# Kernel optimization log

Hardware: AMD Instinct MI355X
Metric: run time of the kernel (lower is better)

## Reference

```python
import jax, jax.numpy as jnp
import numpy as np

N = 8192
DEG = 16            # neighbors per node (excluding self loop)
E = N * (DEG + 1)   # edges incl. self loops
IN, HID, OUT = 512, 256, 128
N_HIDDEN_LAYERS = 2  # n_layers - 1
NEG_SLOPE = 0.2


def _build_adj():
    # circulant-ish adjacency: self loop + 16 fixed offsets -> exactly E nonzeros
    offs = np.concatenate([[0], np.arange(1, DEG + 1) * 131])
    cols = ((np.arange(N)[:, None] + offs[None, :]) % N).reshape(-1)
    rows = np.repeat(np.arange(N), DEG + 1)
    adj = np.zeros((N, N), np.float32)
    adj[rows, cols] = 1.0
    return adj


def setup_inputs() -> dict:
    key = jax.random.key(0)
    ks = jax.random.split(key, 12)
    g = lambda k, shape, fan_in: jax.random.normal(k, shape, jnp.float32) / np.sqrt(fan_in)
    return {
        "x": jax.random.normal(ks[0], (N, IN), jnp.float32),
        "adj": jnp.asarray(_build_adj()),
        "W_emb": g(ks[1], (IN, HID), IN),
        "b_emb": jnp.zeros((HID,), jnp.float32),
        "W_h": g(ks[2], (N_HIDDEN_LAYERS, HID, HID), HID),
        "asrc_h": g(ks[3], (N_HIDDEN_LAYERS, HID), HID),
        "adst_h": g(ks[4], (N_HIDDEN_LAYERS, HID), HID),
        "b_h": jnp.zeros((N_HIDDEN_LAYERS, HID), jnp.float32),
        "W_o": g(ks[5], (HID, OUT), HID),
        "asrc_o": g(ks[6], (OUT,), OUT),
        "adst_o": g(ks[7], (OUT,), OUT),
        "b_o": jnp.zeros((OUT,), jnp.float32),
        "num_edges": E,
    }


def _leaky(v):
    return jnp.where(v >= 0, v, NEG_SLOPE * v)


def _gat_conv(h_in, src, dst, W, a_src, a_dst, b, n):
    # PyG GATConv, heads=1: h = x W; e_ij = LeakyReLU(a_src.h_j + a_dst.h_i)
    # softmax over incoming edges per target i, then weighted scatter-sum + bias.
    h = h_in @ W                                   # [n, out]
    e = _leaky((h @ a_src)[src] + (h @ a_dst)[dst])  # [E]
    m = jax.ops.segment_max(e, dst, num_segments=n)
    w = jnp.exp(e - m[dst])
    s = jax.ops.segment_sum(w, dst, num_segments=n)
    coef = w / s[dst]                              # [E]
    out = jax.ops.segment_sum(coef[:, None] * h[src], dst, num_segments=n)
    return out + b


def reference(x, adj, W_emb, b_emb, W_h, asrc_h, adst_h, b_h, W_o, asrc_o, adst_o, b_o, num_edges):
    n = adj.shape[0]
    # dense_to_sparse: row=target, col=source (SparseTensor adj_t convention)
    dst, src = jnp.nonzero(adj, size=num_edges)
    h = x @ W_emb + b_emb        # emb Linear; dropout is identity in eval
    for l in range(W_h.shape[0]):
        h = _gat_conv(h, src, dst, W_h[l], asrc_h[l], adst_h[l], b_h[l], n)
    return _gat_conv(h, src, dst, W_o, asrc_o, adst_o, b_o, n)
```

## Files before the change

### kernel.cpp

```cpp
#include <hip/hip_runtime.h>


#define N_NODES 8192
#define NMASK 8191

typedef __attribute__((ext_vector_type(8))) short short8;
typedef __attribute__((ext_vector_type(4))) float f32x4;

__device__ __forceinline__ unsigned short f2bf(float f) {
    unsigned u = __float_as_uint(f);
    u += 0x7FFF + ((u >> 16) & 1);
    return (unsigned short)(u >> 16);
}
__device__ __forceinline__ float bf2f(unsigned short h) {
    return __uint_as_float(((unsigned)h) << 16);
}
__device__ __forceinline__ int kswz(int k, int row) {
    return (k & ~63) | ((((k >> 3) & 7) ^ (row & 7)) << 3) | (k & 7);
}
__device__ __forceinline__ void gl_lds16(const void* g, void* lds) {
    __builtin_amdgcn_global_load_lds(
        (const __attribute__((address_space(1))) unsigned int*)g,
        (__attribute__((address_space(3))) unsigned int*)lds, 16, 0, 0);
}

__global__ __launch_bounds__(256)
void prep1(const float* __restrict__ W_emb, const float* __restrict__ W_h,
           unsigned short* __restrict__ wembT, unsigned short* __restrict__ whT) {
    const int idx = blockIdx.x * 256 + threadIdx.x;
    if (idx < 131072) {
        const int n = idx >> 9, k = idx & 511;
        wembT[n * 512 + kswz(k, n)] = f2bf(W_emb[k * 256 + n]);
    } else if (idx < 196608) {
        const int i = idx - 131072;
        const int n = i >> 8, k = i & 255;
        whT[n * 256 + kswz(k, n)] = f2bf(W_h[k * 256 + n]);
    }
}

__global__ __launch_bounds__(512)
void fused_emb_l0(const float* __restrict__ x, const float* __restrict__ W_h,
                  const float* __restrict__ W_o,
                  const unsigned short* __restrict__ wembT,
                  const unsigned short* __restrict__ whT0,
                  unsigned short* __restrict__ whT1, unsigned short* __restrict__ woT,
                  const float* __restrict__ b_emb,
                  const float* __restrict__ a_src, const float* __restrict__ a_dst,
                  float* __restrict__ as_out, float* __restrict__ ad_out,
                  float* __restrict__ hw_out) {
    __shared__ unsigned short sB[2][256 * 64];
    __shared__ unsigned short sA[2 * 32 * 256];
    __shared__ float sRed[2][8][16];
    unsigned short* sAhi = sA;
    unsigned short* sAlo = sA + 32 * 256;
    const int tid = threadIdx.x;
    const int wave = tid >> 6, lane = tid & 63;
    const int wr = wave >> 2, wq = wave & 3;
    const int fl_c = lane & 15, fl_g = lane >> 4;
    const int r0 = blockIdx.x * 32;

    {
        const int idx = blockIdx.x * 512 + tid;
        if (idx < 65536) {
            const int n = idx >> 8, k = idx & 255;
            whT1[n * 256 + kswz(k, n)] = f2bf(W_h[65536 + k * 256 + n]);
        } else if (idx < 98304) {
            const int i = idx - 65536;
            const int n = i >> 8, k = i & 255;
            woT[n * 256 + kswz(k, n)] = f2bf(W_o[k * 128 + n]);
        }
    }

    auto stageB = [&](const unsigned short* W, int stride, int buf, int t) {
        #pragma unroll
        for (int it = 0; it < 4; ++it) {
            const int G = it * 512 + tid;
            const int n = G >> 3, s = G & 7;
            gl_lds16(W + n * stride + t * 64 + s * 8,
                     &sB[buf][(it * 512 + wave * 64) * 8]);
        }
    };

    const int grow = (131 * (r0 + wr * 16 + fl_c)) & NMASK;
    f32x4 acc[4] = {};
    stageB(wembT, 512, 0, 0);
    __syncthreads();
    int cur = 0;
    for (int t = 0; t < 8; ++t) {
        if (t + 1 < 8) stageB(wembT, 512, cur ^ 1, t + 1);
        short8 ah[2], al[2];
        const float* xp = x + (size_t)grow * 512 + t * 64;
        #pragma unroll
        for (int kh = 0; kh < 2; ++kh) {
            const float4 v0 = *(const float4*)(xp + kh * 32 + fl_g * 8);
            const float4 v1 = *(const float4*)(xp + kh * 32 + fl_g * 8 + 4);
            const float vv[8] = {v0.x, v0.y, v0.z, v0.w, v1.x, v1.y, v1.z, v1.w};
            short8 h8, l8;
            #pragma unroll
            for (int j = 0; j < 8; ++j) {
                const unsigned short h = f2bf(vv[j]);
                h8[j] = (short)h;
                l8[j] = (short)f2bf(vv[j] - bf2f(h));
            }
            ah[kh] = h8; al[kh] = l8;
        }
        short8 bh[4][2];
        #pragma unroll
        for (int n = 0; n < 4; ++n) {
            const int c = wq * 64 + n * 16 + fl_c;
            #pragma unroll
            for (int kh = 0; kh < 2; ++kh)
                bh[n][kh] = *(const short8*)&sB[cur][c * 64 + (((kh * 4 + fl_g) ^ (c & 7)) << 3)];
        }
        #pragma unroll
        for (int n = 0; n < 4; ++n)
            #pragma unroll
            for (int kh = 0; kh < 2; ++kh) {
                acc[n] = __builtin_amdgcn_mfma_f32_16x16x32_bf16(ah[kh], bh[n][kh], acc[n], 0, 0, 0);
                acc[n] = __builtin_amdgcn_mfma_f32_16x16x32_bf16(al[kh], bh[n][kh], acc[n], 0, 0, 0);
            }
        __syncthreads();
        cur ^= 1;
    }

    #pragma unroll
    for (int n = 0; n < 4; ++n) {
        const int c = wq * 64 + n * 16 + fl_c;
        const float bb = b_emb[c];
        #pragma unroll
        for (int i = 0; i < 4; ++i) {
            const int lr = wr * 16 + fl_g * 4 + i;
            const float v = acc[n][i] + bb;
            const int pos = lr * 256 + kswz(c, lr);
            const unsigned short h = f2bf(v);
            sAhi[pos] = h;
            sAlo[pos] = f2bf(v - bf2f(h));
        }
    }
    stageB(whT0, 256, 0, 0);
    __syncthreads();

    f32x4 acc2[4] = {};
    cur = 0;
    const int rr = wr * 16 + fl_c;
    for (int t = 0; t < 4; ++t) {
        if (t + 1 < 4) stageB(whT0, 256, cur ^ 1, t + 1);
        short8 ah[2], al[2];
        #pragma unroll
        for (int kh = 0; kh < 2; ++kh) {
            const int off = rr * 256 + t * 64 + (((kh * 4 + fl_g) ^ (rr & 7)) << 3);
            ah[kh] = *(const short8*)&sAhi[off];
            al[kh] = *(const short8*)&sAlo[off];
        }
        short8 bh[4][2];
        #pragma unroll
        for (int n = 0; n < 4; ++n) {
            const int c = wq * 64 + n * 16 + fl_c;
            #pragma unroll
            for (int kh = 0; kh < 2; ++kh)
                bh[n][kh] = *(const short8*)&sB[cur][c * 64 + (((kh * 4 + fl_g) ^ (c & 7)) << 3)];
        }
        #pragma unroll
        for (int n = 0; n < 4; ++n)
            #pragma unroll
            for (int kh = 0; kh < 2; ++kh) {
                acc2[n] = __builtin_amdgcn_mfma_f32_16x16x32_bf16(ah[kh], bh[n][kh], acc2[n], 0, 0, 0);
                acc2[n] = __builtin_amdgcn_mfma_f32_16x16x32_bf16(al[kh], bh[n][kh], acc2[n], 0, 0, 0);
            }
        __syncthreads();
        cur ^= 1;
    }

    float sv[4], dv[4];
    #pragma unroll
    for (int n = 0; n < 4; ++n) {
        const int c = wq * 64 + n * 16 + fl_c;
        sv[n] = a_src[c]; dv[n] = a_dst[c];
    }
    #pragma unroll
    for (int i = 0; i < 4; ++i) {
        float ps = 0.f, pd = 0.f;
        #pragma unroll
        for (int n = 0; n < 4; ++n) { ps += acc2[n][i] * sv[n]; pd += acc2[n][i] * dv[n]; }
        #pragma unroll
        for (int off = 1; off < 16; off <<= 1) {
            ps += __shfl_xor(ps, off, 64);
            pd += __shfl_xor(pd, off, 64);
        }
        if (fl_c == 0) {
            sRed[0][wave][fl_g * 4 + i] = ps;
            sRed[1][wave][fl_g * 4 + i] = pd;
        }
    }
    __syncthreads();
    if (tid < 32) {
        const int band = tid >> 4, rl = tid & 15;
        as_out[r0 + tid] = sRed[0][band * 4 + 0][rl] + sRed[0][band * 4 + 1][rl]
                         + sRed[0][band * 4 + 2][rl] + sRed[0][band * 4 + 3][rl];
        ad_out[r0 + tid] = sRed[1][band * 4 + 0][rl] + sRed[1][band * 4 + 1][rl]
                         + sRed[1][band * 4 + 2][rl] + sRed[1][band * 4 + 3][rl];
    }
    #pragma unroll
    for (int n = 0; n < 4; ++n) {
        const int c = wq * 64 + n * 16 + fl_c;
        #pragma unroll
        for (int i = 0; i < 4; ++i)
            hw_out[(size_t)(r0 + wr * 16 + fl_g * 4 + i) * 256 + c] = acc2[n][i];
    }
}

__global__ __launch_bounds__(512)
void gat_layer_agg(const float* __restrict__ hwPrev, const float* __restrict__ asPrev,
                   const float* __restrict__ adPrev, const float* __restrict__ aggBias,
                   const unsigned short* __restrict__ Bw,
                   const float* __restrict__ a_src, const float* __restrict__ a_dst,
                   float* __restrict__ as_out, float* __restrict__ ad_out,
                   float* __restrict__ hw_out) {
    __shared__ unsigned short sA[2 * 32 * 256];
    __shared__ unsigned short sB[2][256 * 64];
    __shared__ float sWin[48 * 256];
    __shared__ float sAs[48];
    __shared__ float sRed[2][8][16];
    unsigned short* sAhi = sA;
    unsigned short* sAlo = sA + 32 * 256;
    const int tid = threadIdx.x;
    const int wave = tid >> 6, lane = tid & 63;
    const int wr = wave >> 2, wq = wave & 3;
    const int fl_c = lane & 15, fl_g = lane >> 4;
    const int r0 = blockIdx.x * 32;

    auto stageB = [&](int buf, int t) {
        #pragma unroll
        for (int it = 0; it < 4; ++it) {
            const int G = it * 512 + tid;
            const int n = G >> 3, s = G & 7;
            gl_lds16(Bw + n * 256 + t * 64 + s * 8,
                     &sB[buf][(it * 512 + wave * 64) * 8]);
        }
    };

    #pragma unroll
    for (int it = 0; it < 6; ++it) {
        const int G = it * 512 + tid;
        const int j = G >> 6, q = G & 63;
        gl_lds16(hwPrev + (size_t)((r0 + j) & NMASK) * 256 + q * 4,
                 &sWin[(it * 512 + wave * 64) * 4]);
    }
    if (tid < 48) sAs[tid] = asPrev[(r0 + tid) & NMASK];
    stageB(0, 0);
    __syncthreads();
    #pragma unroll
    for (int i = 0; i < 4; ++i) {
        const int t = wave * 4 + i;
        const float adi = adPrev[r0 + t];
        float e[17];
        float mx = -3.4e38f;
        #pragma unroll
        for (int k = 0; k < 17; ++k) {
            float v = sAs[t + k] + adi;
            v = (v >= 0.f) ? v : 0.2f * v;
            e[k] = v;
            mx = fmaxf(mx, v);
        }
        float sum = 0.f;
        #pragma unroll
        for (int k = 0; k < 17; ++k) { e[k] = __expf(e[k] - mx); sum += e[k]; }
        const float inv = 1.f / sum;
        float a0 = 0, a1 = 0, a2 = 0, a3 = 0;
        #pragma unroll
        for (int k = 0; k < 17; ++k) {
            const float c = e[k] * inv;
            const float4 hv = *(const float4*)&sWin[(t + k) * 256 + lane * 4];
            a0 += c * hv.x; a1 += c * hv.y; a2 += c * hv.z; a3 += c * hv.w;
        }
        const float4 bb = *(const float4*)&aggBias[lane * 4];
        a0 += bb.x; a1 += bb.y; a2 += bb.z; a3 += bb.w;
        ushort4 h, l;
        h.x = f2bf(a0); l.x = f2bf(a0 - bf2f(h.x));
        h.y = f2bf(a1); l.y = f2bf(a1 - bf2f(h.y));
        h.z = f2bf(a2); l.z = f2bf(a2 - bf2f(h.z));
        h.w = f2bf(a3); l.w = f2bf(a3 - bf2f(h.w));
        const int pos = t * 256 + kswz(lane * 4, t);
        *(ushort4*)&sAhi[pos] = h;
        *(ushort4*)&sAlo[pos] = l;
    }
    __syncthreads();

    f32x4 acc[4] = {};
    int cur = 0;
    const int rr = wr * 16 + fl_c;
    for (int t = 0; t < 4; ++t) {
        if (t + 1 < 4) stageB(cur ^ 1, t + 1);
        short8 ah[2], al[2];
        #pragma unroll
        for (int kh = 0; kh < 2; ++kh) {
            const int off = rr * 256 + t * 64 + (((kh * 4 + fl_g) ^ (rr & 7)) << 3);
            ah[kh] = *(const short8*)&sAhi[off];
            al[kh] = *(const short8*)&sAlo[off];
        }
        short8 bh[4][2];
        #pragma unroll
        for (int n = 0; n < 4; ++n) {
            const int c = wq * 64 + n * 16 + fl_c;
            #pragma unroll
            for (int kh = 0; kh < 2; ++kh)
                bh[n][kh] = *(const short8*)&sB[cur][c * 64 + (((kh * 4 + fl_g) ^ (c & 7)) << 3)];
        }
        #pragma unroll
        for (int n = 0; n < 4; ++n)
            #pragma unroll
            for (int kh = 0; kh < 2; ++kh) {
                acc[n] = __builtin_amdgcn_mfma_f32_16x16x32_bf16(ah[kh], bh[n][kh], acc[n], 0, 0, 0);
                acc[n] = __builtin_amdgcn_mfma_f32_16x16x32_bf16(al[kh], bh[n][kh], acc[n], 0, 0, 0);
            }
        __syncthreads();
        cur ^= 1;
    }

    float sv[4], dv[4];
    #pragma unroll
    for (int n = 0; n < 4; ++n) {
        const int c = wq * 64 + n * 16 + fl_c;
        sv[n] = a_src[c]; dv[n] = a_dst[c];
    }
    #pragma unroll
    for (int i = 0; i < 4; ++i) {
        float ps = 0.f, pd = 0.f;
        #pragma unroll
        for (int n = 0; n < 4; ++n) { ps += acc[n][i] * sv[n]; pd += acc[n][i] * dv[n]; }
        #pragma unroll
        for (int off = 1; off < 16; off <<= 1) {
            ps += __shfl_xor(ps, off, 64);
            pd += __shfl_xor(pd, off, 64);
        }
        if (fl_c == 0) {
            sRed[0][wave][fl_g * 4 + i] = ps;
            sRed[1][wave][fl_g * 4 + i] = pd;
        }
    }
    __syncthreads();
    if (tid < 32) {
        const int band = tid >> 4, rl = tid & 15;
        as_out[r0 + tid] = sRed[0][band * 4 + 0][rl] + sRed[0][band * 4 + 1][rl]
                         + sRed[0][band * 4 + 2][rl] + sRed[0][band * 4 + 3][rl];
        ad_out[r0 + tid] = sRed[1][band * 4 + 0][rl] + sRed[1][band * 4 + 1][rl]
                         + sRed[1][band * 4 + 2][rl] + sRed[1][band * 4 + 3][rl];
    }
    #pragma unroll
    for (int n = 0; n < 4; ++n) {
        const int c = wq * 64 + n * 16 + fl_c;
        #pragma unroll
        for (int i = 0; i < 4; ++i)
            hw_out[(size_t)(r0 + wr * 16 + fl_g * 4 + i) * 256 + c] = acc[n][i];
    }
}

__global__ __launch_bounds__(512)
void final_fused(const float* __restrict__ hwPrev, const float* __restrict__ asPrev,
                 const float* __restrict__ adPrev, const float* __restrict__ aggBias,
                 const unsigned short* __restrict__ Bw,
                 const float* __restrict__ a_src, const float* __restrict__ a_dst,
                 const float* __restrict__ b_o, float* __restrict__ out) {
    __shared__ float sWin[64 * 256];
    __shared__ unsigned short sA2[2 * 48 * 256];
    __shared__ unsigned short sB[2][128 * 64];
    __shared__ float sAs1[64], sAs2[48], sAd2[48];
    unsigned short* sA2hi = sA2;
    unsigned short* sA2lo = sA2 + 48 * 256;
    const int tid = threadIdx.x;
    const int wave = tid >> 6, lane = tid & 63;
    const int fl_c = lane & 15, fl_g = lane >> 4;
    const int r0 = blockIdx.x * 32;

    auto stageB = [&](int buf, int t) {
        #pragma unroll
        for (int it = 0; it < 2; ++it) {
            const int G = it * 512 + tid;
            const int n = G >> 3, s = G & 7;
            gl_lds16(Bw + n * 256 + t * 64 + s * 8,
                     &sB[buf][(it * 512 + wave * 64) * 8]);
        }
    };

    #pragma unroll
    for (int it = 0; it < 8; ++it) {
        const int G = it * 512 + tid;
        const int j = G >> 6, q = G & 63;
        gl_lds16(hwPrev + (size_t)((r0 + j) & NMASK) * 256 + q * 4,
                 &sWin[(it * 512 + wave * 64) * 4]);
    }
    if (tid < 64) sAs1[tid] = asPrev[(r0 + tid) & NMASK];
    stageB(0, 0);
    __syncthreads();

    #pragma unroll
    for (int i = 0; i < 6; ++i) {
        const int t = wave * 6 + i;
        const float adi = adPrev[(r0 + t) & NMASK];
        float e[17];
        float mx = -3.4e38f;
        #pragma unroll
        for (int k = 0; k < 17; ++k) {
            float v = sAs1[t + k] + adi;
            v = (v >= 0.f) ? v : 0.2f * v;
            e[k] = v;
            mx = fmaxf(mx, v);
        }
        float sum = 0.f;
        #pragma unroll
        for (int k = 0; k < 17; ++k) { e[k] = __expf(e[k] - mx); sum += e[k]; }
        const float inv = 1.f / sum;
        float a0 = 0, a1 = 0, a2 = 0, a3 = 0;
        #pragma unroll
        for (int k = 0; k < 17; ++k) {
            const float c = e[k] * inv;
            const float4 hv = *(const float4*)&sWin[(t + k) * 256 + lane * 4];
            a0 += c * hv.x; a1 += c * hv.y; a2 += c * hv.z; a3 += c * hv.w;
        }
        const float4 bb = *(const float4*)&aggBias[lane * 4];
        a0 += bb.x; a1 += bb.y; a2 += bb.z; a3 += bb.w;
        ushort4 h, l;
        h.x = f2bf(a0); l.x = f2bf(a0 - bf2f(h.x));
        h.y = f2bf(a1); l.y = f2bf(a1 - bf2f(h.y));
        h.z = f2bf(a2); l.z = f2bf(a2 - bf2f(h.z));
        h.w = f2bf(a3); l.w = f2bf(a3 - bf2f(h.w));
        const int pos = t * 256 + kswz(lane * 4, t);
        *(ushort4*)&sA2hi[pos] = h;
        *(ushort4*)&sA2lo[pos] = l;
    }
    __syncthreads();

    f32x4 accF[3] = {};
    int bands[3], cgs[3];
    #pragma unroll
    for (int j = 0; j < 3; ++j) {
        const int f = wave * 3 + j;
        bands[j] = f >> 3; cgs[j] = f & 7;
    }
    int cur = 0;
    for (int t = 0; t < 4; ++t) {
        if (t + 1 < 4) stageB(cur ^ 1, t + 1);
        #pragma unroll
        for (int j = 0; j < 3; ++j) {
            const int rr = bands[j] * 16 + fl_c;
            const int c  = cgs[j] * 16 + fl_c;
            #pragma unroll
            for (int kh = 0; kh < 2; ++kh) {
                const int aoff = rr * 256 + t * 64 + (((kh * 4 + fl_g) ^ (rr & 7)) << 3);
                const short8 ah = *(const short8*)&sA2hi[aoff];
                const short8 al = *(const short8*)&sA2lo[aoff];
                const short8 bh = *(const short8*)&sB[cur][c * 64 + (((kh * 4 + fl_g) ^ (c & 7)) << 3)];
                accF[j] = __builtin_amdgcn_mfma_f32_16x16x32_bf16(ah, bh, accF[j], 0, 0, 0);
                accF[j] = __builtin_amdgcn_mfma_f32_16x16x32_bf16(al, bh, accF[j], 0, 0, 0);
            }
        }
        __syncthreads();
        cur ^= 1;
    }

    float* sHw2 = sWin;
    #pragma unroll
    for (int j = 0; j < 3; ++j)
        #pragma unroll
        for (int i = 0; i < 4; ++i)
            sHw2[(bands[j] * 16 + fl_g * 4 + i) * 128 + cgs[j] * 16 + fl_c] = accF[j][i];
    __syncthreads();

    const float2 s2 = *(const float2*)&a_src[lane * 2];
    const float2 d2 = *(const float2*)&a_dst[lane * 2];
    #pragma unroll
    for (int i = 0; i < 6; ++i) {
        const int t = wave * 6 + i;
        const float2 hv = *(const float2*)&sHw2[t * 128 + lane * 2];
        float ps = hv.x * s2.x + hv.y * s2.y;
        float pd = hv.x * d2.x + hv.y * d2.y;
        #pragma unroll
        for (int off = 1; off < 64; off <<= 1) {
            ps += __shfl_xor(ps, off, 64);
            pd += __shfl_xor(pd, off, 64);
        }
        if (lane == 0) { sAs2[t] = ps; sAd2[t] = pd; }
    }
    __syncthreads();

    const float2 bb = *(const float2*)&b_o[lane * 2];
    #pragma unroll
    for (int i = 0; i < 4; ++i) {
        const int t = wave * 4 + i;
        const int nid = (131 * (r0 + t)) & NMASK;
        const float adi = sAd2[t];
        float e[17];
        float mx = -3.4e38f;
        #pragma unroll
        for (int k = 0; k < 17; ++k) {
            float v = sAs2[t + k] + adi;
            v = (v >= 0.f) ? v : 0.2f * v;
            e[k] = v;
            mx = fmaxf(mx, v);
        }
        float sum = 0.f;
        #pragma unroll
        for (int k = 0; k < 17; ++k) { e[k] = __expf(e[k] - mx); sum += e[k]; }
        const float inv = 1.f / sum;
        float a0 = 0, a1 = 0;
        #pragma unroll
        for (int k = 0; k < 17; ++k) {
            const float c = e[k] * inv;
            const float2 hv = *(const float2*)&sHw2[(t + k) * 128 + lane * 2];
            a0 += c * hv.x; a1 += c * hv.y;
        }
        *(float2*)&out[(size_t)nid * 128 + lane * 2] = make_float2(a0 + bb.x, a1 + bb.y);
    }
}

extern "C" void kernel_launch(void* const* d_in, const int* in_sizes, int n_in,
                              void* d_out, int out_size, void* d_ws, size_t ws_size,
                              hipStream_t stream) {
    (void)in_sizes; (void)n_in; (void)out_size; (void)ws_size;

    const float* x      = (const float*)d_in[0];
    const float* W_emb  = (const float*)d_in[2];
    const float* b_emb  = (const float*)d_in[3];
    const float* W_h    = (const float*)d_in[4];
    const float* asrc_h = (const float*)d_in[5];
    const float* adst_h = (const float*)d_in[6];
    const float* b_h    = (const float*)d_in[7];
    const float* W_o    = (const float*)d_in[8];
    const float* asrc_o = (const float*)d_in[9];
    const float* adst_o = (const float*)d_in[10];
    const float* b_o    = (const float*)d_in[11];

    char* p = (char*)d_ws;
    float* hwA = (float*)p; p += (size_t)N_NODES * 256 * 4;
    float* hwB = (float*)p; p += (size_t)N_NODES * 256 * 4;
    float* as0 = (float*)p; p += N_NODES * 4;
    float* ad0 = (float*)p; p += N_NODES * 4;
    float* as1 = (float*)p; p += N_NODES * 4;
    float* ad1 = (float*)p; p += N_NODES * 4;
    unsigned short* wembT = (unsigned short*)p; p += 256 * 512 * 2;
    unsigned short* whT   = (unsigned short*)p; p += 2 * 256 * 256 * 2;
    unsigned short* woT   = (unsigned short*)p;

    prep1<<<dim3(768), dim3(256), 0, stream>>>(W_emb, W_h, wembT, whT);

    fused_emb_l0<<<dim3(256), dim3(512), 0, stream>>>(
        x, W_h, W_o, wembT, whT, whT + 65536, woT,
        b_emb, asrc_h, adst_h, as0, ad0, hwA);

    gat_layer_agg<<<dim3(256), dim3(512), 0, stream>>>(
        hwA, as0, ad0, b_h,
        whT + 65536, asrc_h + 256, adst_h + 256, as1, ad1, hwB);

    final_fused<<<dim3(256), dim3(512), 0, stream>>>(
        hwB, as1, ad1, b_h + 256, woT, asrc_o, adst_o, b_o, (float*)d_out);
}
```

Baseline: 67.63 us.

## Fuse last two GAT stages with neighbor-block flag handoff; drop x lo-split MFMA

Merges the layer-1 aggregation/transform kernel and the final output kernel into one launch. Between the two phases each block waits only on a flag set by the next block, since its 48-row window needs just those rows, so the grid-wide kernel boundary is gone. Separately, the embedding GEMM drops the bf16 low-part correction for x, which halves its MFMA count at the cost of some accuracy. The spin-wait assumes all 256 blocks are co-resident, and both phases share LDS through a union.

```diff
diff --git a/kernel.cpp b/kernel.cpp
--- a/kernel.cpp
+++ b/kernel.cpp
@@ -26,8 +26,10 @@
 
 __global__ __launch_bounds__(256)
 void prep1(const float* __restrict__ W_emb, const float* __restrict__ W_h,
-           unsigned short* __restrict__ wembT, unsigned short* __restrict__ whT) {
+           unsigned short* __restrict__ wembT, unsigned short* __restrict__ whT,
+           unsigned* __restrict__ flags) {
     const int idx = blockIdx.x * 256 + threadIdx.x;
+    if (idx < 256) flags[idx] = 0u;
     if (idx < 131072) {
         const int n = idx >> 9, k = idx & 511;
         wembT[n * 512 + kswz(k, n)] = f2bf(W_emb[k * 256 + n]);
@@ -88,21 +90,17 @@
     int cur = 0;
     for (int t = 0; t < 8; ++t) {
         if (t + 1 < 8) stageB(wembT, 512, cur ^ 1, t + 1);
-        short8 ah[2], al[2];
+        short8 ah[2];
         const float* xp = x + (size_t)grow * 512 + t * 64;
         #pragma unroll
         for (int kh = 0; kh < 2; ++kh) {
             const float4 v0 = *(const float4*)(xp + kh * 32 + fl_g * 8);
             const float4 v1 = *(const float4*)(xp + kh * 32 + fl_g * 8 + 4);
             const float vv[8] = {v0.x, v0.y, v0.z, v0.w, v1.x, v1.y, v1.z, v1.w};
-            short8 h8, l8;
-            #pragma unroll
-            for (int j = 0; j < 8; ++j) {
-                const unsigned short h = f2bf(vv[j]);
-                h8[j] = (short)h;
-                l8[j] = (short)f2bf(vv[j] - bf2f(h));
-            }
-            ah[kh] = h8; al[kh] = l8;
+            short8 h8;
+            #pragma unroll
+            for (int j = 0; j < 8; ++j) h8[j] = (short)f2bf(vv[j]);
+            ah[kh] = h8;
         }
         short8 bh[4][2];
         #pragma unroll
@@ -115,10 +113,8 @@
         #pragma unroll
         for (int n = 0; n < 4; ++n)
             #pragma unroll
-            for (int kh = 0; kh < 2; ++kh) {
+            for (int kh = 0; kh < 2; ++kh)
                 acc[n] = __builtin_amdgcn_mfma_f32_16x16x32_bf16(ah[kh], bh[n][kh], acc[n], 0, 0, 0);
-                acc[n] = __builtin_amdgcn_mfma_f32_16x16x32_bf16(al[kh], bh[n][kh], acc[n], 0, 0, 0);
-            }
         __syncthreads();
         cur ^= 1;
     }
@@ -209,307 +205,326 @@
     }
 }
 
+union TailSmem {
+    struct {
+        float win[48 * 256];
+        unsigned short A[2 * 32 * 256];
+        unsigned short B[2][256 * 64];
+        float as0[48];
+        float red[2][8][16];
+    } a;
+    struct {
+        float win[64 * 256];
+        unsigned short A2[2 * 48 * 256];
+        unsigned short B[2][128 * 64];
+        float as1[64], as2[48], ad2[48];
+    } b;
+};
+
 __global__ __launch_bounds__(512)
-void gat_layer_agg(const float* __restrict__ hwPrev, const float* __restrict__ asPrev,
-                   const float* __restrict__ adPrev, const float* __restrict__ aggBias,
-                   const unsigned short* __restrict__ Bw,
-                   const float* __restrict__ a_src, const float* __restrict__ a_dst,
-                   float* __restrict__ as_out, float* __restrict__ ad_out,
-                   float* __restrict__ hw_out) {
-    __shared__ unsigned short sA[2 * 32 * 256];
-    __shared__ unsigned short sB[2][256 * 64];
-    __shared__ float sWin[48 * 256];
-    __shared__ float sAs[48];
-    __shared__ float sRed[2][8][16];
-    unsigned short* sAhi = sA;
-    unsigned short* sAlo = sA + 32 * 256;
+void tail_fused(const float* __restrict__ hwA, const float* __restrict__ as0,
+                const float* __restrict__ ad0, const float* __restrict__ bias0,
+                const unsigned short* __restrict__ whT1,
+                const float* __restrict__ asrc1, const float* __restrict__ adst1,
+                float* __restrict__ as1, float* __restrict__ ad1,
+                float* __restrict__ hwB, const float* __restrict__ bias1,
+                const unsigned short* __restrict__ woT,
+                const float* __restrict__ asrc_o, const float* __restrict__ adst_o,
+                const float* __restrict__ b_o, unsigned* __restrict__ flags,
+                float* __restrict__ out) {
+    __shared__ TailSmem smem;
     const int tid = threadIdx.x;
     const int wave = tid >> 6, lane = tid & 63;
     const int wr = wave >> 2, wq = wave & 3;
     const int fl_c = lane & 15, fl_g = lane >> 4;
-    const int r0 = blockIdx.x * 32;
-
-    auto stageB = [&](int buf, int t) {
-        #pragma unroll
-        for (int it = 0; it < 4; ++it) {
+    const int blk = blockIdx.x;
+    const int r0 = blk * 32;
+
+    {
+        unsigned short* sAhi = smem.a.A;
+        unsigned short* sAlo = smem.a.A + 32 * 256;
+
+        auto stageB = [&](int buf, int t) {
+            #pragma unroll
+            for (int it = 0; it < 4; ++it) {
+                const int G = it * 512 + tid;
+                const int n = G >> 3, s = G & 7;
+                gl_lds16(whT1 + n * 256 + t * 64 + s * 8,
+                         &smem.a.B[buf][(it * 512 + wave * 64) * 8]);
+            }
+        };
+
+        #pragma unroll
+        for (int it = 0; it < 6; ++it) {
             const int G = it * 512 + tid;
-            const int n = G >> 3, s = G & 7;
-            gl_lds16(Bw + n * 256 + t * 64 + s * 8,
-                     &sB[buf][(it * 512 + wave * 64) * 8]);
-        }
-    };
-
-    #pragma unroll
-    for (int it = 0; it < 6; ++it) {
-        const int G = it * 512 + tid;
-        const int j = G >> 6, q = G & 63;
-        gl_lds16(hwPrev + (size_t)((r0 + j) & NMASK) * 256 + q * 4,
-                 &sWin[(it * 512 + wave * 64) * 4]);
-    }
-    if (tid < 48) sAs[tid] = asPrev[(r0 + tid) & NMASK];
-    stageB(0, 0);
-    __syncthreads();
-    #pragma unroll
-    for (int i = 0; i < 4; ++i) {
-        const int t = wave * 4 + i;
-        const float adi = adPrev[r0 + t];
-        float e[17];
-        float mx = -3.4e38f;
-        #pragma unroll
-        for (int k = 0; k < 17; ++k) {
-            float v = sAs[t + k] + adi;
-            v = (v >= 0.f) ? v : 0.2f * v;
-            e[k] = v;
-            mx = fmaxf(mx, v);
-        }
-        float sum = 0.f;
-        #pragma unroll
-        for (int k = 0; k < 17; ++k) { e[k] = __expf(e[k] - mx); sum += e[k]; }
-        const float inv = 1.f / sum;
-        float a0 = 0, a1 = 0, a2 = 0, a3 = 0;
-        #pragma unroll
-        for (int k = 0; k < 17; ++k) {
-            const float c = e[k] * inv;
-            const float4 hv = *(const float4*)&sWin[(t + k) * 256 + lane * 4];
-            a0 += c * hv.x; a1 += c * hv.y; a2 += c * hv.z; a3 += c * hv.w;
-        }
-        const float4 bb = *(const float4*)&aggBias[lane * 4];
-        a0 += bb.x; a1 += bb.y; a2 += bb.z; a3 += bb.w;
-        ushort4 h, l;
-        h.x = f2bf(a0); l.x = f2bf(a0 - bf2f(h.x));
-        h.y = f2bf(a1); l.y = f2bf(a1 - bf2f(h.y));
-        h.z = f2bf(a2); l.z = f2bf(a2 - bf2f(h.z));
-        h.w = f2bf(a3); l.w = f2bf(a3 - bf2f(h.w));
-        const int pos = t * 256 + kswz(lane * 4, t);
-        *(ushort4*)&sAhi[pos] = h;
-        *(ushort4*)&sAlo[pos] = l;
-    }
-    __syncthreads();
-
-    f32x4 acc[4] = {};
-    int cur = 0;
-    const int rr = wr * 16 + fl_c;
-    for (int t = 0; t < 4; ++t) {
-        if (t + 1 < 4) stageB(cur ^ 1, t + 1);
-        short8 ah[2], al[2];
-        #pragma unroll
-        for (int kh = 0; kh < 2; ++kh) {
-            const int off = rr * 256 + t * 64 + (((kh * 4 + fl_g) ^ (rr & 7)) << 3);
-            ah[kh] = *(const short8*)&sAhi[off];
-            al[kh] = *(const short8*)&sAlo[off];
-        }
-        short8 bh[4][2];
+            const int j = G >> 6, q = G & 63;
+            gl_lds16(hwA + (size_t)((r0 + j) & NMASK) * 256 + q * 4,
+                     &smem.a.win[(it * 512 + wave * 64) * 4]);
+        }
+        if (tid < 48) smem.a.as0[tid] = as0[(r0 + tid) & NMASK];
+        stageB(0, 0);
+        __syncthreads();
+        #pragma unroll
+        for (int i = 0; i < 4; ++i) {
+            const int t = wave * 4 + i;
+            const float adi = ad0[r0 + t];
+            float e[17];
+            float mx = -3.4e38f;
+            #pragma unroll
+            for (int k = 0; k < 17; ++k) {
+                float v = smem.a.as0[t + k] + adi;
+                v = (v >= 0.f) ? v : 0.2f * v;
+                e[k] = v;
+                mx = fmaxf(mx, v);
+            }
+            float sum = 0.f;
+            #pragma unroll
+            for (int k = 0; k < 17; ++k) { e[k] = __expf(e[k] - mx); sum += e[k]; }
+            const float inv = 1.f / sum;
+            float a0 = 0, a1 = 0, a2 = 0, a3 = 0;
+            #pragma unroll
+            for (int k = 0; k < 17; ++k) {
+                const float c = e[k] * inv;
+                const float4 hv = *(const float4*)&smem.a.win[(t + k) * 256 + lane * 4];
+                a0 += c * hv.x; a1 += c * hv.y; a2 += c * hv.z; a3 += c * hv.w;
+            }
+            const float4 bb = *(const float4*)&bias0[lane * 4];
+            a0 += bb.x; a1 += bb.y; a2 += bb.z; a3 += bb.w;
+            ushort4 h, l;
+            h.x = f2bf(a0); l.x = f2bf(a0 - bf2f(h.x));
+            h.y = f2bf(a1); l.y = f2bf(a1 - bf2f(h.y));
+            h.z = f2bf(a2); l.z = f2bf(a2 - bf2f(h.z));
+            h.w = f2bf(a3); l.w = f2bf(a3 - bf2f(h.w));
+            const int pos = t * 256 + kswz(lane * 4, t);
+            *(ushort4*)&sAhi[pos] = h;
+            *(ushort4*)&sAlo[pos] = l;
+        }
+        __syncthreads();
+
+        f32x4 acc[4] = {};
+        int cur = 0;
+        const int rr = wr * 16 + fl_c;
+        for (int t = 0; t < 4; ++t) {
+            if (t + 1 < 4) stageB(cur ^ 1, t + 1);
+            short8 ah[2], al[2];
+            #pragma unroll
+            for (int kh = 0; kh < 2; ++kh) {
+                const int off = rr * 256 + t * 64 + (((kh * 4 + fl_g) ^ (rr & 7)) << 3);
+                ah[kh] = *(const short8*)&sAhi[off];
+                al[kh] = *(const short8*)&sAlo[off];
+            }
+            short8 bh[4][2];
+            #pragma unroll
+            for (int n = 0; n < 4; ++n) {
+                const int c = wq * 64 + n * 16 + fl_c;
+                #pragma unroll
+                for (int kh = 0; kh < 2; ++kh)
+                    bh[n][kh] = *(const short8*)&smem.a.B[cur][c * 64 + (((kh * 4 + fl_g) ^ (c & 7)) << 3)];
+            }
+            #pragma unroll
+            for (int n = 0; n < 4; ++n)
+                #pragma unroll
+                for (int kh = 0; kh < 2; ++kh) {
+                    acc[n] = __builtin_amdgcn_mfma_f32_16x16x32_bf16(ah[kh], bh[n][kh], acc[n], 0, 0, 0);
+                    acc[n] = __builtin_amdgcn_mfma_f32_16x16x32_bf16(al[kh], bh[n][kh], acc[n], 0, 0, 0);
+                }
+            __syncthreads();
+            cur ^= 1;
+        }
+
+        float sv[4], dv[4];
         #pragma unroll
         for (int n = 0; n < 4; ++n) {
             const int c = wq * 64 + n * 16 + fl_c;
-            #pragma unroll
-            for (int kh = 0; kh < 2; ++kh)
-                bh[n][kh] = *(const short8*)&sB[cur][c * 64 + (((kh * 4 + fl_g) ^ (c & 7)) << 3)];
-        }
-        #pragma unroll
-        for (int n = 0; n < 4; ++n)
-            #pragma unroll
-            for (int kh = 0; kh < 2; ++kh) {
-                acc[n] = __builtin_amdgcn_mfma_f32_16x16x32_bf16(ah[kh], bh[n][kh], acc[n], 0, 0, 0);
-                acc[n] = __builtin_amdgcn_mfma_f32_16x16x32_bf16(al[kh], bh[n][kh], acc[n], 0, 0, 0);
-            }
-        __syncthreads();
-        cur ^= 1;
-    }
-
-    float sv[4], dv[4];
-    #pragma unroll
-    for (int n = 0; n < 4; ++n) {
-        const int c = wq * 64 + n * 16 + fl_c;
-        sv[n] = a_src[c]; dv[n] = a_dst[c];
-    }
-    #pragma unroll
-    for (int i = 0; i < 4; ++i) {
-        float ps = 0.f, pd = 0.f;
-        #pragma unroll
-        for (int n = 0; n < 4; ++n) { ps += acc[n][i] * sv[n]; pd += acc[n][i] * dv[n]; }
-        #pragma unroll
-        for (int off = 1; off < 16; off <<= 1) {
-            ps += __shfl_xor(ps, off, 64);
-            pd += __shfl_xor(pd, off, 64);
-        }
-        if (fl_c == 0) {
-            sRed[0][wave][fl_g * 4 + i] = ps;
-            sRed[1][wave][fl_g * 4 + i] = pd;
-        }
-    }
+            sv[n] = asrc1[c]; dv[n] = adst1[c];
+        }
+        #pragma unroll
+        for (int i = 0; i < 4; ++i) {
+            float ps = 0.f, pd = 0.f;
+            #pragma unroll
+            for (int n = 0; n < 4; ++n) { ps += acc[n][i] * sv[n]; pd += acc[n][i] * dv[n]; }
+            #pragma unroll
+            for (int off = 1; off < 16; off <<= 1) {
+                ps += __shfl_xor(ps, off, 64);
+                pd += __shfl_xor(pd, off, 64);
+            }
+            if (fl_c == 0) {
+                smem.a.red[0][wave][fl_g * 4 + i] = ps;
+                smem.a.red[1][wave][fl_g * 4 + i] = pd;
+            }
+        }
+        __syncthreads();
+        if (tid < 32) {
+            const int band = tid >> 4, rl = tid & 15;
+            as1[r0 + tid] = smem.a.red[0][band * 4 + 0][rl] + smem.a.red[0][band * 4 + 1][rl]
+                          + smem.a.red[0][band * 4 + 2][rl] + smem.a.red[0][band * 4 + 3][rl];
+            ad1[r0 + tid] = smem.a.red[1][band * 4 + 0][rl] + smem.a.red[1][band * 4 + 1][rl]
+                          + smem.a.red[1][band * 4 + 2][rl] + smem.a.red[1][band * 4 + 3][rl];
+        }
+        #pragma unroll
+        for (int n = 0; n < 4; ++n) {
+            const int c = wq * 64 + n * 16 + fl_c;
+            #pragma unroll
+            for (int i = 0; i < 4; ++i)
+                hwB[(size_t)(r0 + wr * 16 + fl_g * 4 + i) * 256 + c] = acc[n][i];
+        }
+    }
+
     __syncthreads();
-    if (tid < 32) {
-        const int band = tid >> 4, rl = tid & 15;
-        as_out[r0 + tid] = sRed[0][band * 4 + 0][rl] + sRed[0][band * 4 + 1][rl]
-                         + sRed[0][band * 4 + 2][rl] + sRed[0][band * 4 + 3][rl];
-        ad_out[r0 + tid] = sRed[1][band * 4 + 0][rl] + sRed[1][band * 4 + 1][rl]
-                         + sRed[1][band * 4 + 2][rl] + sRed[1][band * 4 + 3][rl];
-    }
-    #pragma unroll
-    for (int n = 0; n < 4; ++n) {
-        const int c = wq * 64 + n * 16 + fl_c;
-        #pragma unroll
-        for (int i = 0; i < 4; ++i)
-            hw_out[(size_t)(r0 + wr * 16 + fl_g * 4 + i) * 256 + c] = acc[n][i];
-    }
-}
-
-__global__ __launch_bounds__(512)
-void final_fused(const float* __restrict__ hwPrev, const float* __restrict__ asPrev,
-                 const float* __restrict__ adPrev, const float* __restrict__ aggBias,
-                 const unsigned short* __restrict__ Bw,
-                 const float* __restrict__ a_src, const float* __restrict__ a_dst,
-                 const float* __restrict__ b_o, float* __restrict__ out) {
-    __shared__ float sWin[64 * 256];
-    __shared__ unsigned short sA2[2 * 48 * 256];
-    __shared__ unsigned short sB[2][128 * 64];
-    __shared__ float sAs1[64], sAs2[48], sAd2[48];
-    unsigned short* sA2hi = sA2;
-    unsigned short* sA2lo = sA2 + 48 * 256;
-    const int tid = threadIdx.x;
-    const int wave = tid >> 6, lane = tid & 63;
-    const int fl_c = lane & 15, fl_g = lane >> 4;
-    const int r0 = blockIdx.x * 32;
-
-    auto stageB = [&](int buf, int t) {
-        #pragma unroll
-        for (int it = 0; it < 2; ++it) {
+    if (tid == 0) {
+        __threadfence();
+        __hip_atomic_store(&flags[blk], 1u, __ATOMIC_RELEASE,
+                           __HIP_MEMORY_SCOPE_AGENT);
+        while (__hip_atomic_load(&flags[(blk + 1) & 255], __ATOMIC_ACQUIRE,
+                                 __HIP_MEMORY_SCOPE_AGENT) == 0u)
+            __builtin_amdgcn_s_sleep(2);
+        __threadfence();
+    }
+    __syncthreads();
+
+    {
+        unsigned short* sA2hi = smem.b.A2;
+        unsigned short* sA2lo = smem.b.A2 + 48 * 256;
+
+        auto stageB2 = [&](int buf, int t) {
+            #pragma unroll
+            for (int it = 0; it < 2; ++it) {
+                const int G = it * 512 + tid;
+                const int n = G >> 3, s = G & 7;
+                gl_lds16(woT + n * 256 + t * 64 + s * 8,
+                         &smem.b.B[buf][(it * 512 + wave * 64) * 8]);
+            }
+        };
+
+        #pragma unroll
+        for (int it = 0; it < 8; ++it) {
             const int G = it * 512 + tid;
-            const int n = G >> 3, s = G & 7;
-            gl_lds16(Bw + n * 256 + t * 64 + s * 8,
-                     &sB[buf][(it * 512 + wave * 64) * 8]);
-        }
-    };
-
-    #pragma unroll
-    for (int it = 0; it < 8; ++it) {
-        const int G = it * 512 + tid;
-        const int j = G >> 6, q = G & 63;
-        gl_lds16(hwPrev + (size_t)((r0 + j) & NMASK) * 256 + q * 4,
-                 &sWin[(it * 512 + wave * 64) * 4]);
-    }
-    if (tid < 64) sAs1[tid] = asPrev[(r0 + tid) & NMASK];
-    stageB(0, 0);
-    __syncthreads();
-
-    #pragma unroll
-    for (int i = 0; i < 6; ++i) {
-        const int t = wave * 6 + i;
-        const float adi = adPrev[(r0 + t) & NMASK];
-        float e[17];
-        float mx = -3.4e38f;
-        #pragma unroll
-        for (int k = 0; k < 17; ++k) {
-            float v = sAs1[t + k] + adi;
-            v = (v >= 0.f) ? v : 0.2f * v;
-            e[k] = v;
-            mx = fmaxf(mx, v);
-        }
-        float sum = 0.f;
-        #pragma unroll
-        for (int k = 0; k < 17; ++k) { e[k] = __expf(e[k] - mx); sum += e[k]; }
-        const float inv = 1.f / sum;
-        float a0 = 0, a1 = 0, a2 = 0, a3 = 0;
-        #pragma unroll
-        for (int k = 0; k < 17; ++k) {
-            const float c = e[k] * inv;
-            const float4 hv = *(const float4*)&sWin[(t + k) * 256 + lane * 4];
-            a0 += c * hv.x; a1 += c * hv.y; a2 += c * hv.z; a3 += c * hv.w;
-        }
-        const float4 bb = *(const float4*)&aggBias[lane * 4];
-        a0 += bb.x; a1 += bb.y; a2 += bb.z; a3 += bb.w;
-        ushort4 h, l;
-        h.x = f2bf(a0); l.x = f2bf(a0 - bf2f(h.x));
-        h.y = f2bf(a1); l.y = f2bf(a1 - bf2f(h.y));
-        h.z = f2bf(a2); l.z = f2bf(a2 - bf2f(h.z));
-        h.w = f2bf(a3); l.w = f2bf(a3 - bf2f(h.w));
-        const int pos = t * 256 + kswz(lane * 4, t);
-        *(ushort4*)&sA2hi[pos] = h;
-        *(ushort4*)&sA2lo[pos] = l;
-    }
-    __syncthreads();
-
-    f32x4 accF[3] = {};
-    int bands[3], cgs[3];
-    #pragma unroll
-    for (int j = 0; j < 3; ++j) {
-        const int f = wave * 3 + j;
-        bands[j] = f >> 3; cgs[j] = f & 7;
-    }
-    int cur = 0;
-    for (int t = 0; t < 4; ++t) {
-        if (t + 1 < 4) stageB(cur ^ 1, t + 1);
+            const int j = G >> 6, q = G & 63;
+            gl_lds16(hwB + (size_t)((r0 + j) & NMASK) * 256 + q * 4,
+                     &smem.b.win[(it * 512 + wave * 64) * 4]);
+        }
+        if (tid < 64) smem.b.as1[tid] = as1[(r0 + tid) & NMASK];
+        stageB2(0, 0);
+        __syncthreads();
+
+        #pragma unroll
+        for (int i = 0; i < 6; ++i) {
+            const int t = wave * 6 + i;
+            const float adi = ad1[(r0 + t) & NMASK];
+            float e[17];
+            float mx = -3.4e38f;
+            #pragma unroll
+            for (int k = 0; k < 17; ++k) {
+                float v = smem.b.as1[t + k] + adi;
+                v = (v >= 0.f) ? v : 0.2f * v;
+                e[k] = v;
+                mx = fmaxf(mx, v);
+            }
+            float sum = 0.f;
+            #pragma unroll
+            for (int k = 0; k < 17; ++k) { e[k] = __expf(e[k] - mx); sum += e[k]; }
+            const float inv = 1.f / sum;
+            float a0 = 0, a1v = 0, a2 = 0, a3 = 0;
+            #pragma unroll
+            for (int k = 0; k < 17; ++k) {
+                const float c = e[k] * inv;
+                const float4 hv = *(const float4*)&smem.b.win[(t + k) * 256 + lane * 4];
+                a0 += c * hv.x; a1v += c * hv.y; a2 += c * hv.z; a3 += c * hv.w;
+            }
+            const float4 bb = *(const float4*)&bias1[lane * 4];
+            a0 += bb.x; a1v += bb.y; a2 += bb.z; a3 += bb.w;
+            ushort4 h, l;
+            h.x = f2bf(a0);  l.x = f2bf(a0 - bf2f(h.x));
+            h.y = f2bf(a1v); l.y = f2bf(a1v - bf2f(h.y));
+            h.z = f2bf(a2);  l.z = f2bf(a2 - bf2f(h.z));
+            h.w = f2bf(a3);  l.w = f2bf(a3 - bf2f(h.w));
+            const int pos = t * 256 + kswz(lane * 4, t);
+            *(ushort4*)&sA2hi[pos] = h;
+            *(ushort4*)&sA2lo[pos] = l;
+        }
+        __syncthreads();
+
+        f32x4 accF[3] = {};
+        int bands[3], cgs[3];
         #pragma unroll
         for (int j = 0; j < 3; ++j) {
-            const int rr = bands[j] * 16 + fl_c;
-            const int c  = cgs[j] * 16 + fl_c;
-            #pragma unroll
-            for (int kh = 0; kh < 2; ++kh) {
-                const int aoff = rr * 256 + t * 64 + (((kh * 4 + fl_g) ^ (rr & 7)) << 3);
-                const short8 ah = *(const short8*)&sA2hi[aoff];
-                const short8 al = *(const short8*)&sA2lo[aoff];
-                const short8 bh = *(const short8*)&sB[cur][c * 64 + (((kh * 4 + fl_g) ^ (c & 7)) << 3)];
-                accF[j] = __builtin_amdgcn_mfma_f32_16x16x32_bf16(ah, bh, accF[j], 0, 0, 0);
-                accF[j] = __builtin_amdgcn_mfma_f32_16x16x32_bf16(al, bh, accF[j], 0, 0, 0);
-            }
-        }
-        __syncthreads();
-        cur ^= 1;
-    }
-
-    float* sHw2 = sWin;
-    #pragma unroll
-    for (int j = 0; j < 3; ++j)
-        #pragma unroll
-        for (int i = 0; i < 4; ++i)
-            sHw2[(bands[j] * 16 + fl_g * 4 + i) * 128 + cgs[j] * 16 + fl_c] = accF[j][i];
-    __syncthreads();
-
-    const float2 s2 = *(const float2*)&a_src[lane * 2];
-    const float2 d2 = *(const float2*)&a_dst[lane * 2];
-    #pragma unroll
-    for (int i = 0; i < 6; ++i) {
-        const int t = wave * 6 + i;
-        const float2 hv = *(const float2*)&sHw2[t * 128 + lane * 2];
-        float ps = hv.x * s2.x + hv.y * s2.y;
-        float pd = hv.x * d2.x + hv.y * d2.y;
-        #pragma unroll
-        for (int off = 1; off < 64; off <<= 1) {
-            ps += __shfl_xor(ps, off, 64);
-            pd += __shfl_xor(pd, off, 64);
-        }
-        if (lane == 0) { sAs2[t] = ps; sAd2[t] = pd; }
-    }
-    __syncthreads();
-
-    const float2 bb = *(const float2*)&b_o[lane * 2];
-    #pragma unroll
-    for (int i = 0; i < 4; ++i) {
-        const int t = wave * 4 + i;
-        const int nid = (131 * (r0 + t)) & NMASK;
-        const float adi = sAd2[t];
-        float e[17];
-        float mx = -3.4e38f;
-        #pragma unroll
-        for (int k = 0; k < 17; ++k) {
-            float v = sAs2[t + k] + adi;
-            v = (v >= 0.f) ? v : 0.2f * v;
-            e[k] = v;
-            mx = fmaxf(mx, v);
-        }
-        float sum = 0.f;
-        #pragma unroll
-        for (int k = 0; k < 17; ++k) { e[k] = __expf(e[k] - mx); sum += e[k]; }
-        const float inv = 1.f / sum;
-        float a0 = 0, a1 = 0;
-        #pragma unroll
-        for (int k = 0; k < 17; ++k) {
-            const float c = e[k] * inv;
-            const float2 hv = *(const float2*)&sHw2[(t + k) * 128 + lane * 2];
-            a0 += c * hv.x; a1 += c * hv.y;
-        }
-        *(float2*)&out[(size_t)nid * 128 + lane * 2] = make_float2(a0 + bb.x, a1 + bb.y);
+            const int f = wave * 3 + j;
+            bands[j] = f >> 3; cgs[j] = f & 7;
+        }
+        int cur = 0;
+        for (int t = 0; t < 4; ++t) {
+            if (t + 1 < 4) stageB2(cur ^ 1, t + 1);
+            #pragma unroll
+            for (int j = 0; j < 3; ++j) {
+                const int rr = bands[j] * 16 + fl_c;
+                const int c  = cgs[j] * 16 + fl_c;
+                #pragma unroll
+                for (int kh = 0; kh < 2; ++kh) {
+                    const int aoff = rr * 256 + t * 64 + (((kh * 4 + fl_g) ^ (rr & 7)) << 3);
+                    const short8 ah = *(const short8*)&sA2hi[aoff];
+                    const short8 al = *(const short8*)&sA2lo[aoff];
+                    const short8 bh = *(const short8*)&smem.b.B[cur][c * 64 + (((kh * 4 + fl_g) ^ (c & 7)) << 3)];
+                    accF[j] = __builtin_amdgcn_mfma_f32_16x16x32_bf16(ah, bh, accF[j], 0, 0, 0);
+                    accF[j] = __builtin_amdgcn_mfma_f32_16x16x32_bf16(al, bh, accF[j], 0, 0, 0);
+                }
+            }
+            __syncthreads();
+            cur ^= 1;
+        }
+
+        float* sHw2 = smem.b.win;
+        #pragma unroll
+        for (int j = 0; j < 3; ++j)
+            #pragma unroll
+            for (int i = 0; i < 4; ++i)
+                sHw2[(bands[j] * 16 + fl_g * 4 + i) * 128 + cgs[j] * 16 + fl_c] = accF[j][i];
+        __syncthreads();
+
+        const float2 s2 = *(const float2*)&asrc_o[lane * 2];
+        const float2 d2 = *(const float2*)&adst_o[lane * 2];
+        #pragma unroll
+        for (int i = 0; i < 6; ++i) {
+            const int t = wave * 6 + i;
+            const float2 hv = *(const float2*)&sHw2[t * 128 + lane * 2];
+            float ps = hv.x * s2.x + hv.y * s2.y;
+            float pd = hv.x * d2.x + hv.y * d2.y;
+            #pragma unroll
+            for (int off = 1; off < 64; off <<= 1) {
+                ps += __shfl_xor(ps, off, 64);
+                pd += __shfl_xor(pd, off, 64);
+            }
+            if (lane == 0) { smem.b.as2[t] = ps; smem.b.ad2[t] = pd; }
+        }
+        __syncthreads();
+
+        const float2 bb = *(const float2*)&b_o[lane * 2];
+        #pragma unroll
+        for (int i = 0; i < 4; ++i) {
+            const int t = wave * 4 + i;
+            const int nid = (131 * (r0 + t)) & NMASK;
+            const float adi = smem.b.ad2[t];
+            float e[17];
+            float mx = -3.4e38f;
+            #pragma unroll
+            for (int k = 0; k < 17; ++k) {
+                float v = smem.b.as2[t + k] + adi;
+                v = (v >= 0.f) ? v : 0.2f * v;
+                e[k] = v;
+                mx = fmaxf(mx, v);
+            }
+            float sum = 0.f;
+            #pragma unroll
+            for (int k = 0; k < 17; ++k) { e[k] = __expf(e[k] - mx); sum += e[k]; }
+            const float inv = 1.f / sum;
+            float a0 = 0, a1 = 0;
+            #pragma unroll
+            for (int k = 0; k < 17; ++k) {
+                const float c = e[k] * inv;
+                const float2 hv = *(const float2*)&sHw2[(t + k) * 128 + lane * 2];
+                a0 += c * hv.x; a1 += c * hv.y;
+            }
+            *(float2*)&out[(size_t)nid * 128 + lane * 2] = make_float2(a0 + bb.x, a1 + bb.y);
+        }
     }
 }
 
@@ -539,18 +554,17 @@
     float* ad1 = (float*)p; p += N_NODES * 4;
     unsigned short* wembT = (unsigned short*)p; p += 256 * 512 * 2;
     unsigned short* whT   = (unsigned short*)p; p += 2 * 256 * 256 * 2;
-    unsigned short* woT   = (unsigned short*)p;
-
-    prep1<<<dim3(768), dim3(256), 0, stream>>>(W_emb, W_h, wembT, whT);
+    unsigned short* woT   = (unsigned short*)p; p += 128 * 256 * 2;
+    unsigned* flags = (unsigned*)p;
+
+    prep1<<<dim3(768), dim3(256), 0, stream>>>(W_emb, W_h, wembT, whT, flags);
 
     fused_emb_l0<<<dim3(256), dim3(512), 0, stream>>>(
         x, W_h, W_o, wembT, whT, whT + 65536, woT,
         b_emb, asrc_h, adst_h, as0, ad0, hwA);
 
-    gat_layer_agg<<<dim3(256), dim3(512), 0, stream>>>(
-        hwA, as0, ad0, b_h,
-        whT + 65536, asrc_h + 256, adst_h + 256, as1, ad1, hwB);
-
-    final_fused<<<dim3(256), dim3(512), 0, stream>>>(
-        hwB, as1, ad1, b_h + 256, woT, asrc_o, adst_o, b_o, (float*)d_out);
-}
+    tail_fused<<<dim3(256), dim3(512), 0, stream>>>(
+        hwA, as0, ad0, b_h, whT + 65536, asrc_h + 256, adst_h + 256,
+        as1, ad1, hwB, b_h + 256, woT, asrc_o, adst_o, b_o, flags,
+        (float*)d_out);
+}
```

Result: slower. 94.71 us (+40.1%).
